# Kernel tuning notes

Hardware: AMD Instinct MI355X
Metric: run time of the kernel (lower is better)

The kernel has to match this reference:

```python
import jax, jax.numpy as jnp
import numpy as np

D_MODEL = 1024
N_HEADS = 16
D_K = D_MODEL // N_HEADS


def setup_inputs() -> dict:
    key = jax.random.key(0)
    ks = jax.random.split(key, 11)
    B, S = 2, 2048
    scale = 1.0 / np.sqrt(D_MODEL)
    inp = {
        "q": jax.random.normal(ks[0], (B, S, D_MODEL), jnp.float32),
        "k": jax.random.normal(ks[1], (B, S, D_MODEL), jnp.float32),
        "v": jax.random.normal(ks[2], (B, S, D_MODEL), jnp.float32),
        "W_q": jax.random.normal(ks[3], (D_MODEL, D_MODEL), jnp.float32) * scale,
        "b_q": jnp.zeros((D_MODEL,), jnp.float32),
        "W_k": jax.random.normal(ks[4], (D_MODEL, D_MODEL), jnp.float32) * scale,
        "b_k": jnp.zeros((D_MODEL,), jnp.float32),
        "W_v": jax.random.normal(ks[5], (D_MODEL, D_MODEL), jnp.float32) * scale,
        "b_v": jnp.zeros((D_MODEL,), jnp.float32),
        "W_o": jax.random.normal(ks[6], (D_MODEL, D_MODEL), jnp.float32) * scale,
        "b_o": jnp.zeros((D_MODEL,), jnp.float32),
    }
    return inp


def _split_heads(x):
    B, S, _ = x.shape
    return x.reshape(B, S, N_HEADS, D_K).transpose(0, 2, 1, 3)  # [B,H,S,dk]


def reference(q, k, v, W_q, b_q, W_k, b_k, W_v, b_v, W_o, b_o):
    Q = _split_heads(q @ W_q + b_q)
    K = _split_heads(k @ W_k + b_k)
    V = _split_heads(v @ W_v + b_v)
    scores = jnp.einsum("bhqd,bhkd->bhqk", Q, K) / jnp.sqrt(jnp.float32(D_K))
    attn = jax.nn.softmax(scores, axis=-1)  # [B,H,S,S]
    out = jnp.einsum("bhqk,bhkd->bhqd", attn, V)
    B, H, S, dk = out.shape
    out = out.transpose(0, 2, 1, 3).reshape(B, S, H * dk)
    return out @ W_o + b_o, attn
```

## Files before the change

kernel.cpp:

```cpp
#include <hip/hip_runtime.h>
#include <hip/hip_bf16.h>

typedef __bf16 bf16x8 __attribute__((ext_vector_type(8)));
typedef float f32x4 __attribute__((ext_vector_type(4)));
typedef short short4v __attribute__((ext_vector_type(4)));
typedef unsigned short ushort8v __attribute__((ext_vector_type(8)));

#define DEV static __device__ __forceinline__

#if __has_builtin(__builtin_amdgcn_exp2f)
#define EXP2(x) __builtin_amdgcn_exp2f(x)
#else
#define EXP2(x) exp2f(x)
#endif

DEV unsigned short f2bf(float x) {
  union { __hip_bfloat16 b; unsigned short u; } c;
  c.b = __float2bfloat16(x);
  return c.u;
}

DEV unsigned short f2bf_fast(float x) {
  union { float f; unsigned u; } c;
  c.f = x;
  unsigned u = c.u + 0x7fff + ((c.u >> 16) & 1);
  return (unsigned short)(u >> 16);
}

DEV void gload_lds16(const void* g, void* l) {
  __builtin_amdgcn_global_load_lds((const __attribute__((address_space(1))) void*)g,
                                   (__attribute__((address_space(3))) void*)l, 16, 0, 0);
}

__global__ __launch_bounds__(256) void cvt_qkv(const float* __restrict__ q,
                                               const float* __restrict__ k,
                                               const float* __restrict__ v,
                                               unsigned short* __restrict__ qb,
                                               unsigned short* __restrict__ kb,
                                               unsigned short* __restrict__ vb) {
  const float* src = blockIdx.y == 0 ? q : (blockIdx.y == 1 ? k : v);
  unsigned short* dst = blockIdx.y == 0 ? qb : (blockIdx.y == 1 ? kb : vb);
  int idx = (blockIdx.x * 256 + threadIdx.x) * 4;
  float4 xv = *(const float4*)(src + idx);
  ushort4 o;
  o.x = f2bf(xv.x); o.y = f2bf(xv.y); o.z = f2bf(xv.z); o.w = f2bf(xv.w);
  *(ushort4*)(dst + idx) = o;
}

__global__ __launch_bounds__(256) void transpose_all(const float* __restrict__ W0,
                                                     const float* __restrict__ W1,
                                                     const float* __restrict__ W2,
                                                     const float* __restrict__ W3,
                                                     unsigned short* __restrict__ T0,
                                                     unsigned short* __restrict__ T1,
                                                     unsigned short* __restrict__ T2,
                                                     unsigned short* __restrict__ T3) {
  __shared__ float t[64][68];
  int sel = blockIdx.x >> 8;
  const float* W = sel == 0 ? W0 : sel == 1 ? W1 : sel == 2 ? W2 : W3;
  unsigned short* Wt = sel == 0 ? T0 : sel == 1 ? T1 : sel == 2 ? T2 : T3;
  int tile = blockIdx.x & 255;
  int tr = tile >> 4, tc = tile & 15;
  int lr = threadIdx.x >> 4, lc4 = threadIdx.x & 15;
#pragma unroll
  for (int i = 0; i < 4; ++i) {
    int r = i * 16 + lr;
    float4 v = *(const float4*)(W + (size_t)(tr * 64 + r) * 1024 + tc * 64 + lc4 * 4);
    t[r][lc4 * 4 + 0] = v.x; t[r][lc4 * 4 + 1] = v.y;
    t[r][lc4 * 4 + 2] = v.z; t[r][lc4 * 4 + 3] = v.w;
  }
  __syncthreads();
#pragma unroll
  for (int i = 0; i < 4; ++i) {
    int r = i * 16 + lr;
    ushort4 o;
    o.x = f2bf(t[lc4 * 4 + 0][r]);
    o.y = f2bf(t[lc4 * 4 + 1][r]);
    o.z = f2bf(t[lc4 * 4 + 2][r]);
    o.w = f2bf(t[lc4 * 4 + 3][r]);
    *(ushort4*)(Wt + (size_t)(tc * 64 + r) * 1024 + tr * 64 + lc4 * 4) = o;
  }
}

DEV void gemm_core(const unsigned short* __restrict__ A, const unsigned short* __restrict__ Bt,
                   const float* __restrict__ bias, void* __restrict__ Cout,
                   float scale, int mode, int blk,
                   unsigned short* As, unsigned short* Bs) {
  const int tid = threadIdx.x;
  const int l = tid & 63, w = tid >> 6;
  const int wm = w >> 1, wn = w & 1;
  const int r15 = l & 15, kg = l >> 4;
  const int mt = blk >> 3, nt = blk & 7;

  const f32x4 fz = {0.f, 0.f, 0.f, 0.f};
  f32x4 acc[4][4];
#pragma unroll
  for (int i = 0; i < 4; ++i)
#pragma unroll
    for (int j = 0; j < 4; ++j) acc[i][j] = fz;

  for (int kt = 0; kt < 16; ++kt) {
#pragma unroll
    for (int c = 0; c < 4; ++c) {
      int chunk = c * 256 + tid;
      int row = chunk >> 3, slot = chunk & 7;
      int gsl = slot ^ (row & 7);
      gload_lds16(A + (size_t)(mt * 128 + row) * 1024 + kt * 64 + gsl * 8, As + chunk * 8);
      gload_lds16(Bt + (size_t)(nt * 128 + row) * 1024 + kt * 64 + gsl * 8, Bs + chunk * 8);
    }
    __syncthreads();
#pragma unroll
    for (int ks = 0; ks < 2; ++ks) {
      bf16x8 a[4], b[4];
      int slot = ks * 4 + kg;
#pragma unroll
      for (int i = 0; i < 4; ++i) {
        int ra = wm * 64 + i * 16 + r15;
        a[i] = *(const bf16x8*)(As + ra * 64 + (slot ^ (ra & 7)) * 8);
        int rb = wn * 64 + i * 16 + r15;
        b[i] = *(const bf16x8*)(Bs + rb * 64 + (slot ^ (rb & 7)) * 8);
      }
#pragma unroll
      for (int i = 0; i < 4; ++i)
#pragma unroll
        for (int j = 0; j < 4; ++j)
          acc[i][j] = __builtin_amdgcn_mfma_f32_16x16x32_bf16(a[i], b[j], acc[i][j], 0, 0, 0);
    }
    __syncthreads();
  }

#pragma unroll
  for (int j = 0; j < 4; ++j) {
    int gc = nt * 128 + wn * 64 + j * 16 + r15;
    float bj = bias[gc];
#pragma unroll
    for (int i = 0; i < 4; ++i) {
#pragma unroll
      for (int r = 0; r < 4; ++r) {
        int gr = mt * 128 + wm * 64 + i * 16 + kg * 4 + r;
        float val = (acc[i][j][r] + bj) * scale;
        if (mode == 2) {
          ((float*)Cout)[(size_t)gr * 1024 + gc] = val;
        } else {
          int bb = gr >> 11, s = gr & 2047, hh = gc >> 6, dk = gc & 63;
          if (mode == 0)
            ((unsigned short*)Cout)[((size_t)(bb * 16 + hh) * 2048 + s) * 64 + dk] = f2bf(val);
          else
            ((unsigned short*)Cout)[((size_t)(bb * 16 + hh) * 64 + dk) * 2048 + s] = f2bf(val);
        }
      }
    }
  }
}

__global__ __launch_bounds__(256) void gemm_qkv(const unsigned short* __restrict__ qb,
                                                const unsigned short* __restrict__ kb,
                                                const unsigned short* __restrict__ vb,
                                                const unsigned short* __restrict__ Wtq,
                                                const unsigned short* __restrict__ Wtk,
                                                const unsigned short* __restrict__ Wtv,
                                                const float* __restrict__ bq,
                                                const float* __restrict__ bk,
                                                const float* __restrict__ bv,
                                                unsigned short* __restrict__ Qh,
                                                unsigned short* __restrict__ Kh,
                                                unsigned short* __restrict__ Vt) {
  __shared__ unsigned short As[128 * 64];
  __shared__ unsigned short Bs[128 * 64];
  int sel = blockIdx.x >> 8, blk = blockIdx.x & 255;
  const unsigned short* A = sel == 0 ? qb : sel == 1 ? kb : vb;
  const unsigned short* Bt = sel == 0 ? Wtq : sel == 1 ? Wtk : Wtv;
  const float* bias = sel == 0 ? bq : sel == 1 ? bk : bv;
  void* C = sel == 0 ? (void*)Qh : sel == 1 ? (void*)Kh : (void*)Vt;
  gemm_core(A, Bt, bias, C, sel == 0 ? 0.125f * 1.44269504088896f : 1.0f,
            sel == 2 ? 1 : 0, blk, As, Bs);
}

__global__ __launch_bounds__(256) void gemm_out(const unsigned short* __restrict__ AO,
                                                const unsigned short* __restrict__ Wto,
                                                const float* __restrict__ bo,
                                                float* __restrict__ out0) {
  __shared__ unsigned short As[128 * 64];
  __shared__ unsigned short Bs[128 * 64];
  gemm_core(AO, Wto, bo, out0, 1.0f, 2, blockIdx.x, As, Bs);
}

__global__ __launch_bounds__(256, 4) void attn_kernel(const unsigned short* __restrict__ Qh,
                                                      const unsigned short* __restrict__ Kh,
                                                      const unsigned short* __restrict__ Vt,
                                                      float* __restrict__ attnO,
                                                      unsigned short* __restrict__ AO) {
  __shared__ float Ored[4][32][68];
  __shared__ float Ss[4][32];
  __shared__ float rrow[32];

  const int tid = threadIdx.x;
  const int l = tid & 63, w = tid >> 6;
  const int r15 = l & 15, kg = l >> 4;

  const int lb = ((int)blockIdx.x & 7) * 256 + ((int)blockIdx.x >> 3);
  const int bh = lb >> 6;
  const int q0 = (lb & 63) * 32;
  const int b = bh >> 4, h = bh & 15;

  const unsigned short* Kbase = Kh + (size_t)bh * 2048 * 64;
  const unsigned short* Vbase = Vt + (size_t)bh * 64 * 2048;

  bf16x8 aq[2][2];
#pragma unroll
  for (int j = 0; j < 2; ++j)
#pragma unroll
    for (int h2 = 0; h2 < 2; ++h2)
      aq[j][h2] = *(const bf16x8*)(Qh + ((size_t)bh * 2048 + q0 + j * 16 + r15) * 64 +
                                   (h2 * 4 + kg) * 8);

  const f32x4 z4 = {0.f, 0.f, 0.f, 0.f};
  float s2[2] = {0.f, 0.f};

  {
    const int krow = w * 16 + r15;
    for (int kt = 0; kt < 32; ++kt) {
      const unsigned short* kp = Kbase + (size_t)(kt * 64 + krow) * 64;
      bf16x8 kf0 = *(const bf16x8*)(kp + kg * 8);
      bf16x8 kf1 = *(const bf16x8*)(kp + 32 + kg * 8);
#pragma unroll
      for (int j = 0; j < 2; ++j) {
        f32x4 sc = __builtin_amdgcn_mfma_f32_16x16x32_bf16(kf0, aq[j][0], z4, 0, 0, 0);
        sc = __builtin_amdgcn_mfma_f32_16x16x32_bf16(kf1, aq[j][1], sc, 0, 0, 0);
        s2[j] += EXP2(sc[0]) + EXP2(sc[1]) + EXP2(sc[2]) + EXP2(sc[3]);
      }
    }
  }

#pragma unroll
  for (int j = 0; j < 2; ++j) {
    s2[j] += __shfl_xor(s2[j], 16, 64);
    s2[j] += __shfl_xor(s2[j], 32, 64);
    if (kg == 0) Ss[w][j * 16 + r15] = s2[j];
  }
  __syncthreads();
  if (tid < 32) {
    float s = Ss[0][tid] + Ss[1][tid] + Ss[2][tid] + Ss[3][tid];
    rrow[tid] = 1.0f / s;
  }
  __syncthreads();

  const float rvq[2] = {rrow[r15], rrow[16 + r15]};
  float* attnBase = attnO + ((size_t)bh * 2048 + q0) * 2048;

  f32x4 oacc[2][4];
#pragma unroll
  for (int j = 0; j < 2; ++j)
#pragma unroll
    for (int d = 0; d < 4; ++d) oacc[j][d] = z4;

  f32x4 stv[2][2];
  for (int kt = 0; kt < 16; ++kt) {
    const int cb = kt * 128 + w * 32;
    const unsigned short* kp0 = Kbase + (size_t)(cb + r15) * 64;
    const unsigned short* kp1 = Kbase + (size_t)(cb + 16 + r15) * 64;
    bf16x8 kf00 = *(const bf16x8*)(kp0 + kg * 8);
    bf16x8 kf01 = *(const bf16x8*)(kp0 + 32 + kg * 8);
    bf16x8 kf10 = *(const bf16x8*)(kp1 + kg * 8);
    bf16x8 kf11 = *(const bf16x8*)(kp1 + 32 + kg * 8);
    short4v vf[2][4];
#pragma unroll
    for (int ks = 0; ks < 2; ++ks)
#pragma unroll
      for (int d = 0; d < 4; ++d)
        vf[ks][d] = *(const short4v*)(Vbase + (size_t)(d * 16 + r15) * 2048 + cb + ks * 16 + kg * 4);

    if (kt > 0) {
      const int pb = (kt - 1) * 128 + w * 32;
#pragma unroll
      for (int j = 0; j < 2; ++j)
#pragma unroll
        for (int ks = 0; ks < 2; ++ks)
          *(f32x4*)(attnBase + (size_t)(j * 16 + r15) * 2048 + pb + ks * 16 + kg * 4) = stv[j][ks];
    }

#pragma unroll
    for (int j = 0; j < 2; ++j) {
      {
        f32x4 sc = __builtin_amdgcn_mfma_f32_16x16x32_bf16(kf00, aq[j][0], z4, 0, 0, 0);
        sc = __builtin_amdgcn_mfma_f32_16x16x32_bf16(kf01, aq[j][1], sc, 0, 0, 0);
        float e0 = EXP2(sc[0]), e1 = EXP2(sc[1]), e2 = EXP2(sc[2]), e3 = EXP2(sc[3]);
        f32x4 st = {e0 * rvq[j], e1 * rvq[j], e2 * rvq[j], e3 * rvq[j]};
        stv[j][0] = st;
        short4v pf;
        pf[0] = (short)f2bf_fast(e0); pf[1] = (short)f2bf_fast(e1);
        pf[2] = (short)f2bf_fast(e2); pf[3] = (short)f2bf_fast(e3);
#pragma unroll
        for (int d = 0; d < 4; ++d)
          oacc[j][d] = __builtin_amdgcn_mfma_f32_16x16x16bf16_1k(vf[0][d], pf, oacc[j][d], 0, 0, 0);
      }
      {
        f32x4 sc = __builtin_amdgcn_mfma_f32_16x16x32_bf16(kf10, aq[j][0], z4, 0, 0, 0);
        sc = __builtin_amdgcn_mfma_f32_16x16x32_bf16(kf11, aq[j][1], sc, 0, 0, 0);
        float e0 = EXP2(sc[0]), e1 = EXP2(sc[1]), e2 = EXP2(sc[2]), e3 = EXP2(sc[3]);
        f32x4 st = {e0 * rvq[j], e1 * rvq[j], e2 * rvq[j], e3 * rvq[j]};
        stv[j][1] = st;
        short4v pf;
        pf[0] = (short)f2bf_fast(e0); pf[1] = (short)f2bf_fast(e1);
        pf[2] = (short)f2bf_fast(e2); pf[3] = (short)f2bf_fast(e3);
#pragma unroll
        for (int d = 0; d < 4; ++d)
          oacc[j][d] = __builtin_amdgcn_mfma_f32_16x16x16bf16_1k(vf[1][d], pf, oacc[j][d], 0, 0, 0);
      }
    }
  }
  {
    const int pb = 15 * 128 + w * 32;
#pragma unroll
    for (int j = 0; j < 2; ++j)
#pragma unroll
      for (int ks = 0; ks < 2; ++ks)
        *(f32x4*)(attnBase + (size_t)(j * 16 + r15) * 2048 + pb + ks * 16 + kg * 4) = stv[j][ks];
  }

#pragma unroll
  for (int j = 0; j < 2; ++j)
#pragma unroll
    for (int d = 0; d < 4; ++d)
      *(f32x4*)&Ored[w][j * 16 + r15][d * 16 + kg * 4] = oacc[j][d];
  __syncthreads();
  {
    int q = tid >> 3, dc = (tid & 7) * 8;
    float rv = rrow[q];
    ushort8v o;
#pragma unroll
    for (int i = 0; i < 8; ++i) {
      float s = Ored[0][q][dc + i] + Ored[1][q][dc + i] + Ored[2][q][dc + i] + Ored[3][q][dc + i];
      o[i] = f2bf(s * rv);
    }
    *(ushort8v*)(AO + ((size_t)(b * 2048 + q0 + q)) * 1024 + h * 64 + dc) = o;
  }
}

extern "C" void kernel_launch(void* const* d_in, const int* in_sizes, int n_in,
                              void* d_out, int out_size, void* d_ws, size_t ws_size,
                              hipStream_t stream) {
  const float* q  = (const float*)d_in[0];
  const float* k  = (const float*)d_in[1];
  const float* v  = (const float*)d_in[2];
  const float* Wq = (const float*)d_in[3];
  const float* bq = (const float*)d_in[4];
  const float* Wk = (const float*)d_in[5];
  const float* bk = (const float*)d_in[6];
  const float* Wv = (const float*)d_in[7];
  const float* bvp = (const float*)d_in[8];
  const float* Wo = (const float*)d_in[9];
  const float* bo = (const float*)d_in[10];

  char* wsb = (char*)d_ws;
  const size_t MB = (size_t)1 << 20;
  unsigned short* qb  = (unsigned short*)(wsb + 0 * MB);
  unsigned short* kbp = (unsigned short*)(wsb + 8 * MB);
  unsigned short* vbp = (unsigned short*)(wsb + 16 * MB);
  unsigned short* Wtq = (unsigned short*)(wsb + 24 * MB);
  unsigned short* Wtk = (unsigned short*)(wsb + 26 * MB);
  unsigned short* Wtv = (unsigned short*)(wsb + 28 * MB);
  unsigned short* Wto = (unsigned short*)(wsb + 30 * MB);
  unsigned short* Qh  = (unsigned short*)(wsb + 32 * MB);
  unsigned short* Kh  = (unsigned short*)(wsb + 40 * MB);
  unsigned short* Vt  = (unsigned short*)(wsb + 48 * MB);
  unsigned short* AO  = (unsigned short*)(wsb + 56 * MB);

  float* attnO = (float*)d_out + (size_t)2 * 2048 * 1024;

  cvt_qkv<<<dim3(4096, 3), 256, 0, stream>>>(q, k, v, qb, kbp, vbp);
  transpose_all<<<1024, 256, 0, stream>>>(Wq, Wk, Wv, Wo, Wtq, Wtk, Wtv, Wto);
  gemm_qkv<<<768, 256, 0, stream>>>(qb, kbp, vbp, Wtq, Wtk, Wtv, bq, bk, bvp, Qh, Kh, Vt);
  attn_kernel<<<2048, 256, 0, stream>>>(Qh, Kh, Vt, attnO, AO);
  gemm_out<<<256, 256, 0, stream>>>(AO, Wto, bo, (float*)d_out);
}
```

Before: 429.4 us.

## Split attention into flash PV pass and separate streaming attn-matrix writer

The single attention kernel is split in two. The first computes the row sums and P·V in one pass over K/V, since no max subtraction is needed, and writes out the reciprocal row sums. The second kernel recomputes QK^T and writes the normalized attention matrix with nontemporal stores. This removes the separate row-sum pass from the PV kernel and keeps the large attention-matrix stores out of the MFMA-heavy loop, at the cost of a second kernel launch and recomputing QK^T. rrowG reuses workspace that held qb, which is already consumed by that point.

```diff
diff --git a/kernel.cpp b/kernel.cpp
--- a/kernel.cpp
+++ b/kernel.cpp
@@ -185,11 +185,11 @@
   gemm_core(AO, Wto, bo, out0, 1.0f, 2, blockIdx.x, As, Bs);
 }
 
-__global__ __launch_bounds__(256, 4) void attn_kernel(const unsigned short* __restrict__ Qh,
-                                                      const unsigned short* __restrict__ Kh,
-                                                      const unsigned short* __restrict__ Vt,
-                                                      float* __restrict__ attnO,
-                                                      unsigned short* __restrict__ AO) {
+__global__ __launch_bounds__(256) void attn_flash(const unsigned short* __restrict__ Qh,
+                                                  const unsigned short* __restrict__ Kh,
+                                                  const unsigned short* __restrict__ Vt,
+                                                  unsigned short* __restrict__ AO,
+                                                  float* __restrict__ rrowG) {
   __shared__ float Ored[4][32][68];
   __shared__ float Ss[4][32];
   __shared__ float rrow[32];
@@ -216,19 +216,33 @@
 
   const f32x4 z4 = {0.f, 0.f, 0.f, 0.f};
   float s2[2] = {0.f, 0.f};
-
-  {
-    const int krow = w * 16 + r15;
-    for (int kt = 0; kt < 32; ++kt) {
-      const unsigned short* kp = Kbase + (size_t)(kt * 64 + krow) * 64;
-      bf16x8 kf0 = *(const bf16x8*)(kp + kg * 8);
-      bf16x8 kf1 = *(const bf16x8*)(kp + 32 + kg * 8);
-#pragma unroll
-      for (int j = 0; j < 2; ++j) {
-        f32x4 sc = __builtin_amdgcn_mfma_f32_16x16x32_bf16(kf0, aq[j][0], z4, 0, 0, 0);
-        sc = __builtin_amdgcn_mfma_f32_16x16x32_bf16(kf1, aq[j][1], sc, 0, 0, 0);
-        s2[j] += EXP2(sc[0]) + EXP2(sc[1]) + EXP2(sc[2]) + EXP2(sc[3]);
-      }
+  f32x4 oacc[2][4];
+#pragma unroll
+  for (int j = 0; j < 2; ++j)
+#pragma unroll
+    for (int d = 0; d < 4; ++d) oacc[j][d] = z4;
+
+  const int kb0 = w * 16;
+  for (int kt = 0; kt < 32; ++kt) {
+    const unsigned short* kp = Kbase + (size_t)(kt * 64 + kb0 + r15) * 64;
+    bf16x8 kf0 = *(const bf16x8*)(kp + kg * 8);
+    bf16x8 kf1 = *(const bf16x8*)(kp + 32 + kg * 8);
+    short4v vf[4];
+#pragma unroll
+    for (int d = 0; d < 4; ++d)
+      vf[d] = *(const short4v*)(Vbase + (size_t)(d * 16 + r15) * 2048 + kt * 64 + kb0 + kg * 4);
+#pragma unroll
+    for (int j = 0; j < 2; ++j) {
+      f32x4 sc = __builtin_amdgcn_mfma_f32_16x16x32_bf16(kf0, aq[j][0], z4, 0, 0, 0);
+      sc = __builtin_amdgcn_mfma_f32_16x16x32_bf16(kf1, aq[j][1], sc, 0, 0, 0);
+      float e0 = EXP2(sc[0]), e1 = EXP2(sc[1]), e2 = EXP2(sc[2]), e3 = EXP2(sc[3]);
+      s2[j] += (e0 + e1) + (e2 + e3);
+      short4v pf;
+      pf[0] = (short)f2bf_fast(e0); pf[1] = (short)f2bf_fast(e1);
+      pf[2] = (short)f2bf_fast(e2); pf[3] = (short)f2bf_fast(e3);
+#pragma unroll
+      for (int d = 0; d < 4; ++d)
+        oacc[j][d] = __builtin_amdgcn_mfma_f32_16x16x16bf16_1k(vf[d], pf, oacc[j][d], 0, 0, 0);
     }
   }
 
@@ -241,20 +255,58 @@
   __syncthreads();
   if (tid < 32) {
     float s = Ss[0][tid] + Ss[1][tid] + Ss[2][tid] + Ss[3][tid];
-    rrow[tid] = 1.0f / s;
+    float rv = 1.0f / s;
+    rrow[tid] = rv;
+    rrowG[(size_t)bh * 2048 + q0 + tid] = rv;
   }
   __syncthreads();
 
-  const float rvq[2] = {rrow[r15], rrow[16 + r15]};
+#pragma unroll
+  for (int j = 0; j < 2; ++j)
+#pragma unroll
+    for (int d = 0; d < 4; ++d)
+      *(f32x4*)&Ored[w][j * 16 + r15][d * 16 + kg * 4] = oacc[j][d];
+  __syncthreads();
+  {
+    int q = tid >> 3, dc = (tid & 7) * 8;
+    float rv = rrow[q];
+    ushort8v o;
+#pragma unroll
+    for (int i = 0; i < 8; ++i) {
+      float s = Ored[0][q][dc + i] + Ored[1][q][dc + i] + Ored[2][q][dc + i] + Ored[3][q][dc + i];
+      o[i] = f2bf(s * rv);
+    }
+    *(ushort8v*)(AO + ((size_t)(b * 2048 + q0 + q)) * 1024 + h * 64 + dc) = o;
+  }
+}
+
+__global__ __launch_bounds__(256) void attn_write(const unsigned short* __restrict__ Qh,
+                                                  const unsigned short* __restrict__ Kh,
+                                                  const float* __restrict__ rrowG,
+                                                  float* __restrict__ attnO) {
+  const int tid = threadIdx.x;
+  const int l = tid & 63, w = tid >> 6;
+  const int r15 = l & 15, kg = l >> 4;
+
+  const int lb = ((int)blockIdx.x & 7) * 256 + ((int)blockIdx.x >> 3);
+  const int bh = lb >> 6;
+  const int q0 = (lb & 63) * 32;
+
+  const unsigned short* Kbase = Kh + (size_t)bh * 2048 * 64;
+
+  bf16x8 aq[2][2];
+#pragma unroll
+  for (int j = 0; j < 2; ++j)
+#pragma unroll
+    for (int h2 = 0; h2 < 2; ++h2)
+      aq[j][h2] = *(const bf16x8*)(Qh + ((size_t)bh * 2048 + q0 + j * 16 + r15) * 64 +
+                                   (h2 * 4 + kg) * 8);
+
+  const float rvq[2] = {rrowG[(size_t)bh * 2048 + q0 + r15],
+                        rrowG[(size_t)bh * 2048 + q0 + 16 + r15]};
   float* attnBase = attnO + ((size_t)bh * 2048 + q0) * 2048;
-
-  f32x4 oacc[2][4];
-#pragma unroll
-  for (int j = 0; j < 2; ++j)
-#pragma unroll
-    for (int d = 0; d < 4; ++d) oacc[j][d] = z4;
-
-  f32x4 stv[2][2];
+  const f32x4 z4 = {0.f, 0.f, 0.f, 0.f};
+
   for (int kt = 0; kt < 16; ++kt) {
     const int cb = kt * 128 + w * 32;
     const unsigned short* kp0 = Kbase + (size_t)(cb + r15) * 64;
@@ -263,77 +315,20 @@
     bf16x8 kf01 = *(const bf16x8*)(kp0 + 32 + kg * 8);
     bf16x8 kf10 = *(const bf16x8*)(kp1 + kg * 8);
     bf16x8 kf11 = *(const bf16x8*)(kp1 + 32 + kg * 8);
-    short4v vf[2][4];
-#pragma unroll
-    for (int ks = 0; ks < 2; ++ks)
-#pragma unroll
-      for (int d = 0; d < 4; ++d)
-        vf[ks][d] = *(const short4v*)(Vbase + (size_t)(d * 16 + r15) * 2048 + cb + ks * 16 + kg * 4);
-
-    if (kt > 0) {
-      const int pb = (kt - 1) * 128 + w * 32;
-#pragma unroll
-      for (int j = 0; j < 2; ++j)
-#pragma unroll
-        for (int ks = 0; ks < 2; ++ks)
-          *(f32x4*)(attnBase + (size_t)(j * 16 + r15) * 2048 + pb + ks * 16 + kg * 4) = stv[j][ks];
-    }
-
 #pragma unroll
     for (int j = 0; j < 2; ++j) {
-      {
-        f32x4 sc = __builtin_amdgcn_mfma_f32_16x16x32_bf16(kf00, aq[j][0], z4, 0, 0, 0);
-        sc = __builtin_amdgcn_mfma_f32_16x16x32_bf16(kf01, aq[j][1], sc, 0, 0, 0);
-        float e0 = EXP2(sc[0]), e1 = EXP2(sc[1]), e2 = EXP2(sc[2]), e3 = EXP2(sc[3]);
-        f32x4 st = {e0 * rvq[j], e1 * rvq[j], e2 * rvq[j], e3 * rvq[j]};
-        stv[j][0] = st;
-        short4v pf;
-        pf[0] = (short)f2bf_fast(e0); pf[1] = (short)f2bf_fast(e1);
-        pf[2] = (short)f2bf_fast(e2); pf[3] = (short)f2bf_fast(e3);
-#pragma unroll
-        for (int d = 0; d < 4; ++d)
-          oacc[j][d] = __builtin_amdgcn_mfma_f32_16x16x16bf16_1k(vf[0][d], pf, oacc[j][d], 0, 0, 0);
-      }
-      {
-        f32x4 sc = __builtin_amdgcn_mfma_f32_16x16x32_bf16(kf10, aq[j][0], z4, 0, 0, 0);
-        sc = __builtin_amdgcn_mfma_f32_16x16x32_bf16(kf11, aq[j][1], sc, 0, 0, 0);
-        float e0 = EXP2(sc[0]), e1 = EXP2(sc[1]), e2 = EXP2(sc[2]), e3 = EXP2(sc[3]);
-        f32x4 st = {e0 * rvq[j], e1 * rvq[j], e2 * rvq[j], e3 * rvq[j]};
-        stv[j][1] = st;
-        short4v pf;
-        pf[0] = (short)f2bf_fast(e0); pf[1] = (short)f2bf_fast(e1);
-        pf[2] = (short)f2bf_fast(e2); pf[3] = (short)f2bf_fast(e3);
-#pragma unroll
-        for (int d = 0; d < 4; ++d)
-          oacc[j][d] = __builtin_amdgcn_mfma_f32_16x16x16bf16_1k(vf[1][d], pf, oacc[j][d], 0, 0, 0);
-      }
-    }
-  }
-  {
-    const int pb = 15 * 128 + w * 32;
-#pragma unroll
-    for (int j = 0; j < 2; ++j)
-#pragma unroll
-      for (int ks = 0; ks < 2; ++ks)
-        *(f32x4*)(attnBase + (size_t)(j * 16 + r15) * 2048 + pb + ks * 16 + kg * 4) = stv[j][ks];
-  }
-
-#pragma unroll
-  for (int j = 0; j < 2; ++j)
-#pragma unroll
-    for (int d = 0; d < 4; ++d)
-      *(f32x4*)&Ored[w][j * 16 + r15][d * 16 + kg * 4] = oacc[j][d];
-  __syncthreads();
-  {
-    int q = tid >> 3, dc = (tid & 7) * 8;
-    float rv = rrow[q];
-    ushort8v o;
-#pragma unroll
-    for (int i = 0; i < 8; ++i) {
-      float s = Ored[0][q][dc + i] + Ored[1][q][dc + i] + Ored[2][q][dc + i] + Ored[3][q][dc + i];
-      o[i] = f2bf(s * rv);
-    }
-    *(ushort8v*)(AO + ((size_t)(b * 2048 + q0 + q)) * 1024 + h * 64 + dc) = o;
+      float* rowp = attnBase + (size_t)(j * 16 + r15) * 2048 + cb + kg * 4;
+      f32x4 sc = __builtin_amdgcn_mfma_f32_16x16x32_bf16(kf00, aq[j][0], z4, 0, 0, 0);
+      sc = __builtin_amdgcn_mfma_f32_16x16x32_bf16(kf01, aq[j][1], sc, 0, 0, 0);
+      f32x4 st0 = {EXP2(sc[0]) * rvq[j], EXP2(sc[1]) * rvq[j],
+                   EXP2(sc[2]) * rvq[j], EXP2(sc[3]) * rvq[j]};
+      __builtin_nontemporal_store(st0, (f32x4*)rowp);
+      f32x4 sc1 = __builtin_amdgcn_mfma_f32_16x16x32_bf16(kf10, aq[j][0], z4, 0, 0, 0);
+      sc1 = __builtin_amdgcn_mfma_f32_16x16x32_bf16(kf11, aq[j][1], sc1, 0, 0, 0);
+      f32x4 st1 = {EXP2(sc1[0]) * rvq[j], EXP2(sc1[1]) * rvq[j],
+                   EXP2(sc1[2]) * rvq[j], EXP2(sc1[3]) * rvq[j]};
+      __builtin_nontemporal_store(st1, (f32x4*)(rowp + 16));
+    }
   }
 }
 
@@ -365,12 +360,14 @@
   unsigned short* Kh  = (unsigned short*)(wsb + 40 * MB);
   unsigned short* Vt  = (unsigned short*)(wsb + 48 * MB);
   unsigned short* AO  = (unsigned short*)(wsb + 56 * MB);
+  float* rrowG = (float*)(wsb + 0 * MB);
 
   float* attnO = (float*)d_out + (size_t)2 * 2048 * 1024;
 
   cvt_qkv<<<dim3(4096, 3), 256, 0, stream>>>(q, k, v, qb, kbp, vbp);
   transpose_all<<<1024, 256, 0, stream>>>(Wq, Wk, Wv, Wo, Wtq, Wtk, Wtv, Wto);
   gemm_qkv<<<768, 256, 0, stream>>>(qb, kbp, vbp, Wtq, Wtk, Wtv, bq, bk, bvp, Qh, Kh, Vt);
-  attn_kernel<<<2048, 256, 0, stream>>>(Qh, Kh, Vt, attnO, AO);
+  attn_flash<<<2048, 256, 0, stream>>>(Qh, Kh, Vt, AO, rrowG);
+  attn_write<<<2048, 256, 0, stream>>>(Qh, Kh, rrowG, attnO);
   gemm_out<<<256, 256, 0, stream>>>(AO, Wto, bo, (float*)d_out);
 }
```

Result: slower. 443.9 us (+3.4%).
